# Kernel optimization log

Measured on AMD Instinct MI355X. Metric: run time of the kernel, lower is better.

## Reference

```python
import jax, jax.numpy as jnp
import numpy as np

N_IN, D_IN, N_OUT, D_OUT = 1152, 8, 10, 16
ROUTINGS, NUM_BG = 3, 1
C, H, W = 1, 28, 28
BATCH = 128
DEC_IN = N_OUT * D_OUT  # 160, projection_type=None -> dec_feature_size = outcaps_size


def squash(x, axis=-1):
    norm = jnp.linalg.norm(x, axis=axis, keepdims=True)
    scale = norm ** 2 / (1.0 + norm ** 2) / (norm + 1e-8)
    return scale * x


def scale_coef(x, num_bg):
    # x: [B, n_out] or [B, n_out, n_in]; min/max normalize over dim 1,
    # excluding the last num_bg (background) capsules, then floor at 0.5.
    if num_bg > 0:
        xm = x[:, : x.shape[1] - num_bg]
    else:
        xm = x
    mn = jnp.min(xm, axis=1, keepdims=True)
    mx = jnp.max(xm, axis=1, keepdims=True)
    out = (xm - mn) / jnp.maximum(mx - mn, 1e-6)  # vrange (0,1)
    if num_bg > 0:
        out = jnp.concatenate([out, jnp.zeros_like(out[:, :num_bg])], axis=1)
    return jnp.maximum(out, 0.5)


def decode(capsflat, W1, b1, W2, b2, W3, b3):
    # fcn decoder (eval mode: dropout is identity): 160 -> 512 -> 1024 -> C*H*W
    h = jax.nn.relu(capsflat @ W1 + b1)
    h = jax.nn.relu(h @ W2 + b2)
    return jax.nn.sigmoid(h @ W3 + b3)


def setup_inputs() -> dict:
    key = jax.random.key(0)
    ks = jax.random.split(key, 9)
    return {
        'incaps': jax.random.normal(ks[0], (BATCH, N_IN, D_IN), jnp.float32),
        'x_input': jax.random.uniform(ks[1], (BATCH, C, H, W), jnp.float32),
        'weight': 0.1 * jax.random.normal(ks[2], (N_OUT, N_IN, D_OUT, D_IN), jnp.float32),
        'W1': 0.05 * jax.random.normal(ks[3], (DEC_IN, 512), jnp.float32),
        'b1': jnp.zeros((512,), jnp.float32),
        'W2': 0.05 * jax.random.normal(ks[4], (512, 1024), jnp.float32),
        'b2': jnp.zeros((1024,), jnp.float32),
        'W3': 0.05 * jax.random.normal(ks[5], (1024, C * H * W), jnp.float32),
        'b3': jnp.zeros((C * H * W,), jnp.float32),
    }


def reference(incaps, x_input, weight, W1, b1, W2, b2, W3, b3):
    B = incaps.shape[0]
    # outcaps_hat: matmul(weight, incaps[:,None,:,:,None]).squeeze(-1)
    hat = jnp.einsum('nkoi,bki->bnko', weight, incaps)  # [B, n_out, n_in, d_out]
    hat_d = jax.lax.stop_gradient(hat)
    rc = jnp.ones((B, N_OUT, N_IN), hat.dtype)
    eye = jnp.eye(N_OUT, dtype=hat.dtype)
    x_flat = x_input.reshape(B, 1, -1)
    for _ in range(ROUTINGS - 1):
        # squash over capsule dim, weighted sum over input capsules
        outcaps = squash(jnp.sum(rc[..., None] * hat_d, axis=2, keepdims=True))  # [B,n,1,d]
        b = jnp.sum(outcaps * hat_d, axis=-1)  # agreement [B, n_out, n_in]
        c = scale_coef(b, NUM_BG)
        objcaps = outcaps[:, :, 0, :]  # [B, n_out, d_out]
        # get_every_obj_rscore vectorized: mask one object capsule at a time
        masked = objcaps[:, None, :, :] * eye[None, :, :, None]  # [B, n_obj, n_out, d]
        recon = decode(masked.reshape(B, N_OUT, DEC_IN), W1, b1, W2, b2, W3, b3)  # [B,n_obj,CHW]
        rscore = -jnp.sum((x_flat - recon) ** 2, axis=-1)  # neg MSE-sum, [B, n_obj]
        r = scale_coef(rscore, NUM_BG)
        rc = c * r[:, :, None]
    # final iteration uses non-detached hat
    outcaps = squash(jnp.sum(rc[..., None] * hat, axis=2, keepdims=True))
    return outcaps[:, :, 0, :]  # [B, n_out, d_out]
```

## Files before the change

kernel.cpp:

```cpp
#include <hip/hip_runtime.h>
#include <math.h>

#define BATCH  128
#define NIN    1152
#define DIN    8
#define NOUTC  10
#define DOUT   16
#define H1DIM  512
#define H2DIM  1024
#define PIX    784
#define NROWS  (BATCH * NOUTC)
#define NBY3   13

typedef __attribute__((ext_vector_type(8))) __bf16 bf16x8;
typedef __attribute__((ext_vector_type(4))) float  f32x4;
typedef __attribute__((ext_vector_type(4))) unsigned int u32x4;

__device__ __forceinline__ float bf2f(unsigned int u) {
    union { unsigned int i; float f; } v; v.i = u << 16; return v.f;
}
__device__ __forceinline__ ushort f2bf(float f) {
    union { float f; unsigned int i; } v; v.f = f;
    unsigned int r = v.i + 0x7FFFu + ((v.i >> 16) & 1u);
    return (ushort)(r >> 16);
}
__device__ __forceinline__ float ldin(const void* p, size_t i, int isbf) {
    return isbf ? bf2f(((const ushort*)p)[i]) : ((const float*)p)[i];
}
__device__ __forceinline__ bf16x8 frag_of(uint4 u) {
    return __builtin_bit_cast(bf16x8, u);
}
__device__ __forceinline__ bf16x8 ld_frag(const ushort* p) {
    return frag_of(*(const uint4*)p);
}
__device__ __forceinline__ void unpack8(uint4 u, float* f) {
    f[0] = bf2f(u.x & 0xffffu); f[1] = bf2f(u.x >> 16);
    f[2] = bf2f(u.y & 0xffffu); f[3] = bf2f(u.y >> 16);
    f[4] = bf2f(u.z & 0xffffu); f[5] = bf2f(u.z >> 16);
    f[6] = bf2f(u.w & 0xffffu); f[7] = bf2f(u.w >> 16);
}

__device__ __forceinline__ int detect_bf(const void* w, int* cntS) {
    int tid = threadIdx.x, nt = blockDim.x;
    if (tid == 0) *cntS = 0;
    __syncthreads();
    const ushort* u = (const ushort*)w;
    int c = 0;
    for (int s = tid; s < 512; s += nt) {
        int e = (u[s * 2] >> 7) & 0xFF;
        if (e >= 88 && e <= 140) c++;
    }
    atomicAdd(cntS, c);
    __syncthreads();
    return (*cntS >= 384) ? 1 : 0;
}

struct PrepArgs {
    const void* w;
    const void* src[7];
    ushort*     dst[7];
    int         n[7];
    int*        flag;
};

__global__ __launch_bounds__(256) void prep_kernel(PrepArgs a)
{
    __shared__ int cntS;
    __shared__ ushort tile[32][33];
    int tid = threadIdx.x;
    int isbf = detect_bf(a.w, &cntS);
    int seg = blockIdx.y;
    if (seg == 0 && blockIdx.x == 0 && tid == 0) *a.flag = isbf;

    if (seg <= 4) {
        int n = a.n[seg];
        int stride = gridDim.x * 256;
        ushort* d = a.dst[seg];
        if (isbf) {
            const ushort* s = (const ushort*)a.src[seg];
            for (int i = blockIdx.x * 256 + tid; i < n; i += stride) d[i] = s[i];
        } else {
            const float* s = (const float*)a.src[seg];
            for (int i = blockIdx.x * 256 + tid; i < n; i += stride) d[i] = f2bf(s[i]);
        }
        return;
    }
    int R = (seg == 5) ? H1DIM : H2DIM;
    int C = (seg == 5) ? H2DIM : PIX;
    int tilesX = (seg == 5) ? 32 : 25;
    int tilesY = (seg == 5) ? 16 : 32;
    int t = blockIdx.x;
    if (t >= tilesX * tilesY) return;
    int tx2 = t % tilesX, ty2 = t / tilesX;
    int c0 = tx2 * 32, r0 = ty2 * 32;
    const void* in = a.src[seg];
    ushort* out = a.dst[seg];
    int tx = tid & 31, ty = tid >> 5;
    for (int i = ty; i < 32; i += 8) {
        int r = r0 + i, c = c0 + tx;
        tile[i][tx] = (r < R && c < C) ? f2bf(ldin(in, (size_t)r * C + c, isbf)) : (ushort)0;
    }
    __syncthreads();
    for (int i = ty; i < 32; i += 8) {
        int c = c0 + i, r = r0 + tx;
        if (c < C && r < R) out[(size_t)c * R + r] = tile[tx][i];
    }
}

__global__ __launch_bounds__(256) void hat_prep_kernel(
    const void* __restrict__ inc,
    PrepArgs a,
    ushort* __restrict__ hatG)
{
    __shared__ int cntS;
    __shared__ ushort tile[32][33];
    int tid = threadIdx.x;
    int isbf = detect_bf(a.w, &cntS);

    if (blockIdx.z >= NOUTC) {
        int p = (blockIdx.z - NOUTC) * 144 + blockIdx.y * 9 + blockIdx.x;
        if (p == 0 && tid == 0) *a.flag = isbf;
        if (p < 528) {
            for (int t = p; t < 1312; t += 528) {
                int seg = (t < 512) ? 5 : 6;
                int tt  = (seg == 5) ? t : t - 512;
                int R = (seg == 5) ? H1DIM : H2DIM;
                int C = (seg == 5) ? H2DIM : PIX;
                int tilesX = (seg == 5) ? 32 : 25;
                int tx2 = tt % tilesX, ty2 = tt / tilesX;
                int c0 = tx2 * 32, r0 = ty2 * 32;
                const void* in = a.src[seg];
                ushort* out = a.dst[seg];
                int tx = tid & 31, ty = tid >> 5;
                for (int i = ty; i < 32; i += 8) {
                    int r = r0 + i, c = c0 + tx;
                    tile[i][tx] = (r < R && c < C) ? f2bf(ldin(in, (size_t)r * C + c, isbf)) : (ushort)0;
                }
                __syncthreads();
                for (int i = ty; i < 32; i += 8) {
                    int c = c0 + i, r = r0 + tx;
                    if (c < C && r < R) out[(size_t)c * R + r] = tile[tx][i];
                }
                __syncthreads();
            }
        } else {
            int base = (p - 528) * 256 + tid;
            const int stride = 48 * 256;
            #pragma unroll
            for (int seg = 0; seg <= 4; seg++) {
                int n = a.n[seg];
                ushort* d = a.dst[seg];
                if (isbf) {
                    const ushort* s = (const ushort*)a.src[seg];
                    for (int i = base; i < n; i += stride) d[i] = s[i];
                } else {
                    const float* s = (const float*)a.src[seg];
                    for (int i = base; i < n; i += stride) d[i] = f2bf(s[i]);
                }
            }
        }
        return;
    }

    int kc = blockIdx.x, bc = blockIdx.y, n = blockIdx.z;
    int k  = kc * 128 + (tid >> 1);
    int oh = (tid & 1) << 3;
    int b0 = bc * 8;

    size_t wbase = ((size_t)n * NIN + k) * DOUT + oh;

    if (isbf) {
        uint4 wr[8], ir[8];
        const uint4* wp = (const uint4*)((const ushort*)a.w + wbase * DIN);
        const ushort* ip = (const ushort*)inc;
        #pragma unroll
        for (int j = 0; j < 8; j++) wr[j] = wp[j];
        #pragma unroll
        for (int bl = 0; bl < 8; bl++)
            ir[bl] = *(const uint4*)(ip + ((size_t)(b0 + bl) * NIN + k) * DIN);
        float wf[8][8];
        #pragma unroll
        for (int j = 0; j < 8; j++) unpack8(wr[j], wf[j]);
        #pragma unroll
        for (int bl = 0; bl < 8; bl++) {
            float xi[8];
            unpack8(ir[bl], xi);
            unsigned int hh[8];
            #pragma unroll
            for (int j = 0; j < 8; j++) {
                float s = wf[j][0] * xi[0] + wf[j][1] * xi[1] + wf[j][2] * xi[2] +
                          wf[j][3] * xi[3] + wf[j][4] * xi[4] + wf[j][5] * xi[5] +
                          wf[j][6] * xi[6] + wf[j][7] * xi[7];
                hh[j] = f2bf(s);
            }
            u32x4 ov = { hh[0] | (hh[1] << 16), hh[2] | (hh[3] << 16),
                         hh[4] | (hh[5] << 16), hh[6] | (hh[7] << 16) };
            *(u32x4*)(hatG + (((size_t)((b0 + bl) * NOUTC + n) * NIN + k) * DOUT + oh)) = ov;
        }
    } else {
        float4 wlo[8], whi[8], ilo[8], ihi[8];
        const float4* wp = (const float4*)((const float*)a.w + wbase * DIN);
        const float*  ip = (const float*)inc;
        #pragma unroll
        for (int j = 0; j < 8; j++) { wlo[j] = wp[2 * j]; whi[j] = wp[2 * j + 1]; }
        #pragma unroll
        for (int bl = 0; bl < 8; bl++) {
            const float4* q = (const float4*)(ip + ((size_t)(b0 + bl) * NIN + k) * DIN);
            ilo[bl] = q[0]; ihi[bl] = q[1];
        }
        #pragma unroll
        for (int bl = 0; bl < 8; bl++) {
            float4 lo = ilo[bl], hi = ihi[bl];
            unsigned int hh[8];
            #pragma unroll
            for (int j = 0; j < 8; j++) {
                float s = wlo[j].x * lo.x + wlo[j].y * lo.y + wlo[j].z * lo.z +
                          wlo[j].w * lo.w + whi[j].x * hi.x + whi[j].y * hi.y +
                          whi[j].z * hi.z + whi[j].w * hi.w;
                hh[j] = f2bf(s);
            }
            u32x4 ov = { hh[0] | (hh[1] << 16), hh[2] | (hh[3] << 16),
                         hh[4] | (hh[5] << 16), hh[6] | (hh[7] << 16) };
            *(u32x4*)(hatG + (((size_t)((b0 + bl) * NOUTC + n) * NIN + k) * DOUT + oh)) = ov;
        }
    }
}

struct MegaArgs {
    const ushort* hatG;
    const ushort* W1c; const ushort* b1c;
    const ushort* W2T; const ushort* b2c;
    const ushort* W3T; const ushort* b3c;
    const ushort* xc;
    ushort* h1; ushort* h2;
    ushort* bsA; ushort* bsB;
    float*  partials;
    void*   outFinal;
    const int* flagp;
};

union MegaSmem {
    struct { uint4 As4[640]; uint4 Bs4[640]; } g;
    struct { ushort wSb[NIN]; float redS[4][16]; float sumS[16];
             float ocS[16]; float scaleS; } r;
};

__device__ __forceinline__ void red_item(
    const MegaArgs& A, MegaSmem& S, int bn, int notFirst,
    const ushort* bsPrev, ushort* bsOut, ushort* h1out, int writeOut)
{
    int n = bn % NOUTC, b = bn / NOUTC;
    int t = threadIdx.x;
    int wave = t >> 6, lane = t & 63;
    const ushort* hbase = A.hatG + (size_t)bn * NIN * DOUT;

    uint4 v[4][2];
    #pragma unroll
    for (int j = 0; j < 4; j++) {
        v[j][0] = *(const uint4*)(hbase + (t + 256 * j) * DOUT);
        v[j][1] = *(const uint4*)(hbase + (t + 256 * j) * DOUT + 8);
    }
    uint4 vt0 = make_uint4(0,0,0,0), vt1 = make_uint4(0,0,0,0);
    if (t < 128) {
        vt0 = *(const uint4*)(hbase + (1024 + t) * DOUT);
        vt1 = *(const uint4*)(hbase + (1024 + t) * DOUT + 8);
    }

    if (notFirst) {
        if (t < 9) {
            float s = 0.f;
            #pragma unroll
            for (int j = 0; j < NBY3; j++)
                s += A.partials[(size_t)(b * NOUTC + t) * 16 + j];
            S.r.sumS[t] = -s;
        }
        __syncthreads();
        float mn = 1e30f, mx = -1e30f;
        #pragma unroll
        for (int n2 = 0; n2 < 9; n2++) {
            float vv = S.r.sumS[n2];
            mn = fminf(mn, vv); mx = fmaxf(mx, vv);
        }
        float den = fmaxf(mx - mn, 1e-6f);
        float rv = (n < 9) ? fmaxf((S.r.sumS[n] - mn) / den, 0.5f) : 0.5f;
        __syncthreads();
        for (int k = t; k < NIN; k += 256) {
            float c = 0.5f;
            if (n < 9) {
                float vv[9], mn2 = 1e30f, mx2 = -1e30f;
                #pragma unroll
                for (int n2 = 0; n2 < 9; n2++) {
                    vv[n2] = bf2f(bsPrev[(size_t)(b * NOUTC + n2) * NIN + k]);
                    mn2 = fminf(mn2, vv[n2]); mx2 = fmaxf(mx2, vv[n2]);
                }
                float den2 = fmaxf(mx2 - mn2, 1e-6f);
                c = fmaxf((vv[n] - mn2) / den2, 0.5f);
            }
            S.r.wSb[k] = f2bf(c * rv);
        }
    }
    __syncthreads();

    float acc[16];
    #pragma unroll
    for (int o = 0; o < 16; o++) acc[o] = 0.f;
    #pragma unroll
    for (int j = 0; j < 4; j++) {
        int k = t + 256 * j;
        float w = notFirst ? bf2f(S.r.wSb[k]) : 1.f;
        bf16x8 h0 = frag_of(v[j][0]), h1v = frag_of(v[j][1]);
        #pragma unroll
        for (int o = 0; o < 8; o++) {
            acc[o]     += w * (float)h0[o];
            acc[8 + o] += w * (float)h1v[o];
        }
    }
    if (t < 128) {
        float w = notFirst ? bf2f(S.r.wSb[1024 + t]) : 1.f;
        bf16x8 h0 = frag_of(vt0), h1v = frag_of(vt1);
        #pragma unroll
        for (int o = 0; o < 8; o++) {
            acc[o]     += w * (float)h0[o];
            acc[8 + o] += w * (float)h1v[o];
        }
    }
    #pragma unroll
    for (int off = 32; off >= 1; off >>= 1) {
        #pragma unroll
        for (int o = 0; o < 16; o++) acc[o] += __shfl_xor(acc[o], off);
    }
    if (lane == 0) {
        #pragma unroll
        for (int o = 0; o < 16; o++) S.r.redS[wave][o] = acc[o];
    }
    __syncthreads();
    if (t < 16) {
        float s = 0.f;
        #pragma unroll
        for (int wv = 0; wv < 4; wv++) s += S.r.redS[wv][t];
        S.r.sumS[t] = s;
    }
    __syncthreads();
    if (t == 0) {
        float n2 = 0.f;
        #pragma unroll
        for (int o = 0; o < 16; o++) n2 += S.r.sumS[o] * S.r.sumS[o];
        float nrm = sqrtf(n2);
        S.r.scaleS = n2 / (1.f + n2) / (nrm + 1e-8f);
    }
    __syncthreads();
    if (t < 16) {
        float oc = S.r.scaleS * S.r.sumS[t];
        S.r.ocS[t] = oc;
        if (writeOut) {
            if (*A.flagp) ((ushort*)A.outFinal)[(size_t)bn * 16 + t] = f2bf(oc);
            else          ((float*) A.outFinal)[(size_t)bn * 16 + t] = oc;
        }
    }
    __syncthreads();

    if (bsOut) {
        float oc[16];
        #pragma unroll
        for (int o = 0; o < 16; o++) oc[o] = S.r.ocS[o];
        #pragma unroll
        for (int j = 0; j < 4; j++) {
            bf16x8 h0 = frag_of(v[j][0]), h1v = frag_of(v[j][1]);
            float s = 0.f;
            #pragma unroll
            for (int o = 0; o < 8; o++)
                s += oc[o] * (float)h0[o] + oc[8 + o] * (float)h1v[o];
            bsOut[(size_t)bn * NIN + t + 256 * j] = f2bf(s);
        }
        if (t < 128) {
            bf16x8 h0 = frag_of(vt0), h1v = frag_of(vt1);
            float s = 0.f;
            #pragma unroll
            for (int o = 0; o < 8; o++)
                s += oc[o] * (float)h0[o] + oc[8 + o] * (float)h1v[o];
            bsOut[(size_t)bn * NIN + 1024 + t] = f2bf(s);
        }
    }
    if (h1out) {
        #pragma unroll
        for (int cc = 0; cc < 2; cc++) {
            int col = t + 256 * cc;
            float acc1 = bf2f(A.b1c[col]);
            #pragma unroll
            for (int i = 0; i < 16; i++)
                acc1 += S.r.ocS[i] * bf2f(A.W1c[(size_t)(n * 16 + i) * H1DIM + col]);
            h1out[(size_t)bn * H1DIM + col] = f2bf(fmaxf(acc1, 0.f));
        }
    }
}

__device__ __forceinline__ void gemm_tile(
    MegaSmem& S, const ushort* __restrict__ A_, const ushort* __restrict__ Bt,
    const ushort* __restrict__ bias, int K, int N,
    ushort* __restrict__ Cout, const ushort* __restrict__ xin,
    float* __restrict__ partials, int m0, int n0, int tileY)
{
    int tid = threadIdx.x;
    int wave = tid >> 6, lane = tid & 63, quad = lane >> 4, l16 = lane & 15;
    uint4* As4 = S.g.As4;
    uint4* Bs4 = S.g.Bs4;
    ushort* As = (ushort*)As4;
    ushort* Bs = (ushort*)Bs4;

    f32x4 acc[4];
    #pragma unroll
    for (int nt = 0; nt < 4; nt++)
        #pragma unroll
        for (int rg = 0; rg < 4; rg++) acc[nt][rg] = 0.f;

    int sMi = tid >> 2, sKk = (tid & 3) * 8;
    int sLds = sMi * 5 + (tid & 3);
    const ushort* Ap = A_ + (size_t)(m0 + sMi) * K + sKk;
    const ushort* Bp = Bt + (size_t)(n0 + sMi) * K + sKk;
    bool bOK = (n0 + sMi) < N;

    uint4 aR0 = *(const uint4*)Ap;
    uint4 aR1 = *(const uint4*)(Ap + 32);
    uint4 bR0 = bOK ? *(const uint4*)Bp : make_uint4(0, 0, 0, 0);
    uint4 bR1 = bOK ? *(const uint4*)(Bp + 32) : make_uint4(0, 0, 0, 0);

    for (int k0 = 0; k0 < K; k0 += 64) {
        As4[sLds]       = aR0;
        As4[320 + sLds] = aR1;
        Bs4[sLds]       = bR0;
        Bs4[320 + sLds] = bR1;
        __syncthreads();
        if (k0 + 64 < K) {
            aR0 = *(const uint4*)(Ap + k0 + 64);
            aR1 = *(const uint4*)(Ap + k0 + 96);
            bR0 = bOK ? *(const uint4*)(Bp + k0 + 64) : make_uint4(0, 0, 0, 0);
            bR1 = bOK ? *(const uint4*)(Bp + k0 + 96) : make_uint4(0, 0, 0, 0);
        }
        #pragma unroll
        for (int c = 0; c < 2; c++) {
            bf16x8 a = ld_frag(As + c * 2560 + (wave * 16 + l16) * 40 + quad * 8);
            #pragma unroll
            for (int nt = 0; nt < 4; nt++) {
                bf16x8 bb = ld_frag(Bs + c * 2560 + (nt * 16 + l16) * 40 + quad * 8);
                acc[nt] = __builtin_amdgcn_mfma_f32_16x16x32_bf16(a, bb, acc[nt], 0, 0, 0);
            }
        }
        __syncthreads();
    }

    int rowBase = m0 + wave * 16 + quad * 4;
    if (Cout) {
        #pragma unroll
        for (int nt = 0; nt < 4; nt++) {
            int col = n0 + nt * 16 + l16;
            float bv = bf2f(bias[col]);
            #pragma unroll
            for (int rg = 0; rg < 4; rg++) {
                float v = acc[nt][rg] + bv;
                Cout[(size_t)(rowBase + rg) * N + col] = f2bf(fmaxf(v, 0.f));
            }
        }
    } else {
        float vr[4] = {0.f, 0.f, 0.f, 0.f};
        #pragma unroll
        for (int nt = 0; nt < 4; nt++) {
            int col = n0 + nt * 16 + l16;
            if (col < N) {
                float bv = bf2f(bias[col]);
                #pragma unroll
                for (int rg = 0; rg < 4; rg++) {
                    int row = rowBase + rg;
                    int bb = row / NOUTC;
                    float z = acc[nt][rg] + bv;
                    float s = 1.f / (1.f + __expf(-z));
                    float d = bf2f(xin[(size_t)bb * PIX + col]) - s;
                    vr[rg] += d * d;
                }
            }
        }
        #pragma unroll
        for (int rg = 0; rg < 4; rg++) {
            float v = vr[rg];
            #pragma unroll
            for (int off = 8; off >= 1; off >>= 1) v += __shfl_xor(v, off, 16);
            if (l16 == 0)
                partials[(size_t)(rowBase + rg) * 16 + tileY] = v;
        }
    }
}

__global__ __launch_bounds__(256) void red_pass256(MegaArgs A, int mode)
{
    __shared__ MegaSmem S;
    if (mode == 0)      red_item(A, S, blockIdx.x, 0, nullptr, A.bsA, A.h1, 0);
    else if (mode == 1) red_item(A, S, blockIdx.x, 1, A.bsA, A.bsB, A.h1, 0);
    else                red_item(A, S, blockIdx.x, 1, A.bsB, nullptr, nullptr, 1);
}

__global__ __launch_bounds__(256) void gemm_kernel(
    const ushort* __restrict__ A, const ushort* __restrict__ Bt,
    const ushort* __restrict__ bias, int K, int N,
    ushort* __restrict__ Cout,
    const ushort* __restrict__ xin, float* __restrict__ partials)
{
    __shared__ MegaSmem S;
    gemm_tile(S, A, Bt, bias, K, N, Cout, xin, partials,
              blockIdx.x * 64, blockIdx.y * 64, blockIdx.y);
}

__global__ __launch_bounds__(512, 4) void reduce_compute(
    const void*   __restrict__ incRaw,
    const void*   __restrict__ wRaw,
    const ushort* __restrict__ bsPrev,
    const float*  __restrict__ partials,
    int iter0,
    const ushort* __restrict__ W1c,
    const ushort* __restrict__ b1c,
    ushort* __restrict__ h1out,
    ushort* __restrict__ bsOut,
    void*   __restrict__ outFinal,
    const int* __restrict__ flagp)
{
    int bn  = blockIdx.x;
    int n   = bn % NOUTC;
    int b   = bn / NOUTC;
    int tid = threadIdx.x;

    __shared__ ushort wSb[NIN];
    __shared__ float  redS[8][16];
    __shared__ float  sumS[16];
    __shared__ float  ocS[16];
    __shared__ float  scaleS;

    int h = tid & 1, kb = tid >> 1;
    int wave = tid >> 6, lane = tid & 63;

    uint4 v[4];
    const ushort* tailS;

    __shared__ int cntS;
    __shared__ uint4 hatS4[NIN * DOUT / 8];
    int isbf = detect_bf(wRaw, &cntS);
    size_t wnb = (size_t)n * NIN * DOUT * DIN;
    for (int idx = tid; idx < NIN * DOUT; idx += 512) {
        int k = idx >> 4;
        float s = 0.f;
        #pragma unroll
        for (int i = 0; i < 8; i++)
            s += ldin(wRaw, wnb + (size_t)idx * 8 + i, isbf) *
                 ldin(incRaw, ((size_t)b * NIN + k) * DIN + i, isbf);
        ((ushort*)hatS4)[idx] = f2bf(s);
    }
    __syncthreads();
    const ushort* hbase = (const ushort*)hatS4;
    #pragma unroll
    for (int j = 0; j < 4; j++)
        v[j] = *(const uint4*)(hbase + ((kb + 256 * j) * DOUT + h * 8));
    tailS = hbase + 1024 * DOUT;

    if (!iter0) {
        if (tid < 9) {
            float s = 0.f;
            #pragma unroll
            for (int j = 0; j < NBY3; j++)
                s += partials[(size_t)(b * NOUTC + tid) * 16 + j];
            sumS[tid] = -s;
        }
        __syncthreads();
        float mn = 1e30f, mx = -1e30f;
        #pragma unroll
        for (int n2 = 0; n2 < 9; n2++) {
            float vv = sumS[n2];
            mn = fminf(mn, vv); mx = fmaxf(mx, vv);
        }
        float den = fmaxf(mx - mn, 1e-6f);
        float rv = (n < 9) ? fmaxf((sumS[n] - mn) / den, 0.5f) : 0.5f;
        for (int k = tid; k < NIN; k += 512) {
            float c = 0.5f;
            if (n < 9) {
                float vv[9], mn2 = 1e30f, mx2 = -1e30f;
                #pragma unroll
                for (int n2 = 0; n2 < 9; n2++) {
                    vv[n2] = bf2f(bsPrev[(size_t)(b * NOUTC + n2) * NIN + k]);
                    mn2 = fminf(mn2, vv[n2]); mx2 = fmaxf(mx2, vv[n2]);
                }
                float den2 = fmaxf(mx2 - mn2, 1e-6f);
                c = fmaxf((vv[n] - mn2) / den2, 0.5f);
            }
            wSb[k] = f2bf(c * rv);
        }
    }
    __syncthreads();

    float acc[8];
    #pragma unroll
    for (int o = 0; o < 8; o++) acc[o] = 0.f;
    #pragma unroll
    for (int j = 0; j < 4; j++) {
        int k = kb + 256 * j;
        float w = iter0 ? 1.f : bf2f(wSb[k]);
        bf16x8 hv = frag_of(v[j]);
        #pragma unroll
        for (int o = 0; o < 8; o++) acc[o] += w * (float)hv[o];
    }
    if (tid < 256) {
        int k = 1024 + kb;
        float w = iter0 ? 1.f : bf2f(wSb[k]);
        bf16x8 hv = ld_frag(tailS + kb * DOUT + h * 8);
        #pragma unroll
        for (int o = 0; o < 8; o++) acc[o] += w * (float)hv[o];
    }
    #pragma unroll
    for (int off = 32; off >= 2; off >>= 1) {
        #pragma unroll
        for (int o = 0; o < 8; o++) acc[o] += __shfl_xor(acc[o], off);
    }
    if (lane < 2) {
        #pragma unroll
        for (int o = 0; o < 8; o++) redS[wave][lane * 8 + o] = acc[o];
    }
    __syncthreads();
    if (tid < 16) {
        float s = 0.f;
        #pragma unroll
        for (int wv = 0; wv < 8; wv++) s += redS[wv][tid];
        sumS[tid] = s;
    }
    __syncthreads();
    if (tid == 0) {
        float n2 = 0.f;
        #pragma unroll
        for (int o = 0; o < 16; o++) n2 += sumS[o] * sumS[o];
        float nrm = sqrtf(n2);
        scaleS = n2 / (1.f + n2) / (nrm + 1e-8f);
    }
    __syncthreads();
    if (tid < 16) {
        float oc = scaleS * sumS[tid];
        ocS[tid] = oc;
        if (outFinal) {
            if (*flagp) ((ushort*)outFinal)[(size_t)bn * 16 + tid] = f2bf(oc);
            else        ((float*) outFinal)[(size_t)bn * 16 + tid] = oc;
        }
    }
    __syncthreads();

    if (bsOut) {
        float o0 = ocS[h * 8 + 0], o1 = ocS[h * 8 + 1], o2 = ocS[h * 8 + 2],
              o3 = ocS[h * 8 + 3], o4 = ocS[h * 8 + 4], o5 = ocS[h * 8 + 5],
              o6 = ocS[h * 8 + 6], o7 = ocS[h * 8 + 7];
        #pragma unroll
        for (int j = 0; j < 4; j++) {
            bf16x8 hv = frag_of(v[j]);
            float s = o0 * (float)hv[0] + o1 * (float)hv[1] + o2 * (float)hv[2] +
                      o3 * (float)hv[3] + o4 * (float)hv[4] + o5 * (float)hv[5] +
                      o6 * (float)hv[6] + o7 * (float)hv[7];
            s += __shfl_xor(s, 1);
            if (h == 0) bsOut[(size_t)bn * NIN + kb + 256 * j] = f2bf(s);
        }
        if (tid < 256) {
            bf16x8 hv = ld_frag(tailS + kb * DOUT + h * 8);
            float s = o0 * (float)hv[0] + o1 * (float)hv[1] + o2 * (float)hv[2] +
                      o3 * (float)hv[3] + o4 * (float)hv[4] + o5 * (float)hv[5] +
                      o6 * (float)hv[6] + o7 * (float)hv[7];
            s += __shfl_xor(s, 1);
            if (h == 0) bsOut[(size_t)bn * NIN + 1024 + kb] = f2bf(s);
        }
    }

    if (h1out) {
        int col = tid;
        float acc1 = bf2f(b1c[col]);
        #pragma unroll
        for (int i = 0; i < 16; i++)
            acc1 += ocS[i] * bf2f(W1c[(size_t)(n * 16 + i) * H1DIM + col]);
        h1out[(size_t)bn * H1DIM + col] = f2bf(fmaxf(acc1, 0.f));
    }
}

extern "C" void kernel_launch(void* const* d_in, const int* in_sizes, int n_in,
                              void* d_out, int out_size, void* d_ws, size_t ws_size,
                              hipStream_t stream)
{
    const void* inc = d_in[0];
    const void* x   = d_in[1];
    const void* w   = d_in[2];
    const void* W1  = d_in[3];
    const void* b1  = d_in[4];
    const void* W2  = d_in[5];
    const void* b2  = d_in[6];
    const void* W3  = d_in[7];
    const void* b3  = d_in[8];

    char* p = (char*)d_ws;
    auto alloc = [&](size_t bytes) { void* r = p; p += (bytes + 255) & ~(size_t)255; return r; };
    int*    flagWS    = (int*)alloc(256);
    ushort* bsA       = (ushort*)alloc((size_t)NROWS * NIN * 2);
    ushort* bsB       = (ushort*)alloc((size_t)NROWS * NIN * 2);
    float*  partials  = (float*)alloc((size_t)NROWS * 16 * 4);
    ushort* h1WS      = (ushort*)alloc((size_t)NROWS * H1DIM * 2);
    ushort* h2WS      = (ushort*)alloc((size_t)NROWS * H2DIM * 2);
    ushort* W2T       = (ushort*)alloc((size_t)H2DIM * H1DIM * 2);
    ushort* W3T       = (ushort*)alloc((size_t)PIX * H2DIM * 2);
    ushort* W1c       = (ushort*)alloc((size_t)160 * H1DIM * 2);
    ushort* b1c       = (ushort*)alloc((size_t)H1DIM * 2);
    ushort* b2c       = (ushort*)alloc((size_t)H2DIM * 2);
    ushort* b3c       = (ushort*)alloc((size_t)PIX * 2);
    ushort* xc        = (ushort*)alloc((size_t)BATCH * PIX * 2);
    ushort* hatG      = (ushort*)alloc((size_t)NROWS * NIN * DOUT * 2);
    bool haveHat = ((char*)hatG + (size_t)NROWS * NIN * DOUT * 2) <= ((char*)d_ws + ws_size);

    PrepArgs pa;
    pa.w = w;
    pa.src[0] = W1;  pa.dst[0] = W1c;  pa.n[0] = 160 * H1DIM;
    pa.src[1] = b1;  pa.dst[1] = b1c;  pa.n[1] = H1DIM;
    pa.src[2] = b2;  pa.dst[2] = b2c;  pa.n[2] = H2DIM;
    pa.src[3] = b3;  pa.dst[3] = b3c;  pa.n[3] = PIX;
    pa.src[4] = x;   pa.dst[4] = xc;   pa.n[4] = BATCH * PIX;
    pa.src[5] = W2;  pa.dst[5] = W2T;  pa.n[5] = 0;
    pa.src[6] = W3;  pa.dst[6] = W3T;  pa.n[6] = 0;
    pa.flag = flagWS;

    if (!haveHat) {
        prep_kernel<<<dim3(800, 7), 256, 0, stream>>>(pa);
        reduce_compute<<<NROWS, 512, 0, stream>>>(
            inc, w, nullptr, nullptr, 1, W1c, b1c, h1WS, bsA, nullptr, flagWS);
        for (int it = 0; it < 2; it++) {
            gemm_kernel<<<dim3(NROWS / 64, H2DIM / 64), 256, 0, stream>>>(
                h1WS, W2T, b2c, H1DIM, H2DIM, h2WS, nullptr, nullptr);
            gemm_kernel<<<dim3(NROWS / 64, NBY3), 256, 0, stream>>>(
                h2WS, W3T, b3c, H2DIM, PIX, nullptr, xc, partials);
            int last = (it == 1);
            const ushort* bsP = (it == 0) ? bsA : bsB;
            ushort* bsO       = last ? nullptr : bsB;
            ushort* h1o       = last ? nullptr : h1WS;
            void*   fin       = last ? d_out : nullptr;
            reduce_compute<<<NROWS, 512, 0, stream>>>(
                inc, w, bsP, partials, 0, W1c, b1c, h1o, bsO, fin, flagWS);
        }
        return;
    }

    hat_prep_kernel<<<dim3(9, 16, NOUTC + 4), 256, 0, stream>>>(inc, pa, hatG);

    MegaArgs ma;
    ma.hatG = hatG; ma.W1c = W1c; ma.b1c = b1c;
    ma.W2T = W2T;   ma.b2c = b2c; ma.W3T = W3T; ma.b3c = b3c;
    ma.xc = xc;     ma.h1 = h1WS; ma.h2 = h2WS;
    ma.bsA = bsA;   ma.bsB = bsB; ma.partials = partials;
    ma.outFinal = d_out; ma.flagp = flagWS;

    red_pass256<<<NROWS, 256, 0, stream>>>(ma, 0);
    for (int it = 0; it < 2; it++) {
        gemm_kernel<<<dim3(NROWS / 64, H2DIM / 64), 256, 0, stream>>>(
            h1WS, W2T, b2c, H1DIM, H2DIM, h2WS, nullptr, nullptr);
        gemm_kernel<<<dim3(NROWS / 64, NBY3), 256, 0, stream>>>(
            h2WS, W3T, b3c, H2DIM, PIX, nullptr, xc, partials);
        red_pass256<<<NROWS, 256, 0, stream>>>(ma, (it == 0) ? 1 : 2);
    }
}
```

Before: 197.6 us.

## Fuse routing reduce and decoder GEMMs into one dataflow kernel per iteration

Replaces the per-iteration sequence of reduce, two GEMM launches and the next reduce with a single fused_iter kernel. Every block first runs a reduce item, and some blocks run a second one. Blocks then wait on global atomic counters per 64-row group before running the W2 and W3 GEMM tiles. This is meant to cut launch overhead and the full-grid barriers between stages, so GEMM tiles can start as soon as their input rows are ready. The cost is spin-waiting and uneven work per block, and it depends on producer blocks being resident so the waits cannot deadlock.

Measured after the change: 526.7 us. +166.6%, slower.

```diff
diff --git a/kernel.cpp b/kernel.cpp
--- a/kernel.cpp
+++ b/kernel.cpp
@@ -61,6 +61,7 @@
     ushort*     dst[7];
     int         n[7];
     int*        flag;
+    int*        sync;
 };
 
 __global__ __launch_bounds__(256) void prep_kernel(PrepArgs a)
@@ -119,7 +120,10 @@
 
     if (blockIdx.z >= NOUTC) {
         int p = (blockIdx.z - NOUTC) * 144 + blockIdx.y * 9 + blockIdx.x;
-        if (p == 0 && tid == 0) *a.flag = isbf;
+        if (p == 0) {
+            if (tid == 0) *a.flag = isbf;
+            if (tid < 128) a.sync[tid] = 0;
+        }
         if (p < 528) {
             for (int t = p; t < 1312; t += 528) {
                 int seg = (t < 512) ? 5 : 6;
@@ -489,6 +493,55 @@
     }
 }
 
+__device__ __forceinline__ void signal_cnt(int* cnt) {
+    __syncthreads();
+    if (threadIdx.x == 0) { __threadfence(); atomicAdd(cnt, 1); }
+}
+__device__ __forceinline__ void wait_cnt(int* cnt, int target) {
+    if (threadIdx.x == 0) {
+        while (atomicAdd(cnt, 0) < target) __builtin_amdgcn_s_sleep(1);
+        __threadfence();
+    }
+    __syncthreads();
+}
+
+__global__ __launch_bounds__(256, 4) void fused_iter(
+    MegaArgs A, int* cnt1, int* cnt2, int redMode)
+{
+    __shared__ MegaSmem S;
+    int bid = blockIdx.x;
+    int tid = threadIdx.x;
+
+    {
+        int bn = bid;
+        if (redMode == 0) red_item(A, S, bn, 0, nullptr, A.bsA, A.h1, 0);
+        else              red_item(A, S, bn, 1, A.bsA, A.bsB, A.h1, 0);
+        signal_cnt(&cnt1[bn >> 6]);
+    }
+    if (bid >= 580 && bid < 836) {
+        int bn = 1024 + (bid - 580);
+        __syncthreads();
+        if (redMode == 0) red_item(A, S, bn, 0, nullptr, A.bsA, A.h1, 0);
+        else              red_item(A, S, bn, 1, A.bsA, A.bsB, A.h1, 0);
+        signal_cnt(&cnt1[bn >> 6]);
+        return;
+    }
+
+    if (bid < 320) {
+        int m0 = bid % 20, n0v = bid / 20;
+        wait_cnt(&cnt1[m0], 64);
+        gemm_tile(S, A.h1, A.W2T, A.b2c, H1DIM, H2DIM, A.h2,
+                  nullptr, nullptr, m0 * 64, n0v * 64, 0);
+        signal_cnt(&cnt2[m0]);
+    } else if (bid < 580) {
+        int u = bid - 320;
+        int m0 = u % 20, cy = u / 20;
+        wait_cnt(&cnt2[m0], 16);
+        gemm_tile(S, A.h2, A.W3T, A.b3c, H2DIM, PIX, nullptr,
+                  A.xc, A.partials, m0 * 64, cy * 64, cy);
+    }
+}
+
 __global__ __launch_bounds__(256) void red_pass256(MegaArgs A, int mode)
 {
     __shared__ MegaSmem S;
@@ -695,6 +748,7 @@
     char* p = (char*)d_ws;
     auto alloc = [&](size_t bytes) { void* r = p; p += (bytes + 255) & ~(size_t)255; return r; };
     int*    flagWS    = (int*)alloc(256);
+    int*    syncWS    = (int*)alloc(128 * sizeof(int));
     ushort* bsA       = (ushort*)alloc((size_t)NROWS * NIN * 2);
     ushort* bsB       = (ushort*)alloc((size_t)NROWS * NIN * 2);
     float*  partials  = (float*)alloc((size_t)NROWS * 16 * 4);
@@ -720,6 +774,7 @@
     pa.src[5] = W2;  pa.dst[5] = W2T;  pa.n[5] = 0;
     pa.src[6] = W3;  pa.dst[6] = W3T;  pa.n[6] = 0;
     pa.flag = flagWS;
+    pa.sync = syncWS;
 
     if (!haveHat) {
         prep_kernel<<<dim3(800, 7), 256, 0, stream>>>(pa);
@@ -750,12 +805,7 @@
     ma.bsA = bsA;   ma.bsB = bsB; ma.partials = partials;
     ma.outFinal = d_out; ma.flagp = flagWS;
 
-    red_pass256<<<NROWS, 256, 0, stream>>>(ma, 0);
-    for (int it = 0; it < 2; it++) {
-        gemm_kernel<<<dim3(NROWS / 64, H2DIM / 64), 256, 0, stream>>>(
-            h1WS, W2T, b2c, H1DIM, H2DIM, h2WS, nullptr, nullptr);
-        gemm_kernel<<<dim3(NROWS / 64, NBY3), 256, 0, stream>>>(
-            h2WS, W3T, b3c, H2DIM, PIX, nullptr, xc, partials);
-        red_pass256<<<NROWS, 256, 0, stream>>>(ma, (it == 0) ? 1 : 2);
-    }
-}
+    fused_iter<<<1024, 256, 0, stream>>>(ma, syncWS + 0,  syncWS + 20, 0);
+    fused_iter<<<1024, 256, 0, stream>>>(ma, syncWS + 64, syncWS + 84, 1);
+    red_pass256<<<NROWS, 256, 0, stream>>>(ma, 2);
+}
```
